# Kernel tuning notes

Measured on AMD Instinct MI355X. Metric: run time of the kernel, lower is better.

The kernel has to match this reference:

```python
import jax, jax.numpy as jnp
import numpy as np

B, PLEN, D = 32, 1024, 256


def setup_inputs() -> dict:
    key = jax.random.key(0)
    ks = jax.random.split(key, 8)
    u = lambda k, shape: jax.random.uniform(k, shape, jnp.float32, -0.05, 0.05)
    return {
        "P": jax.random.normal(ks[0], (B, PLEN, D), jnp.float32),
        "w_itr_att": u(ks[1], (3 * D,)),
        "w1": u(ks[2], (2 * D, D)),
        "w2": u(ks[3], (2 * D, D)),
        "w3": u(ks[4], (2 * D, D)),
        "b1": u(ks[5], (D,)),
        "b2": u(ks[6], (D,)),
        "b3": u(ks[7], (D,)),
    }


def reference(P, w_itr_att, w1, w2, w3, b1, b2, b3):
    d = P.shape[-1]
    # alpha(a,b) = w_itr_att . [a ; b ; a*b]; split w into the three d-chunks
    wa, wb, wc = w_itr_att[:d], w_itr_att[d:2 * d], w_itr_att[2 * d:]
    # pairwise score A[b,i,j] = wa.P_i + wb.P_j + wc.(P_i * P_j)
    sa = P @ wa                                   # (b, p)
    sb = P @ wb                                   # (b, p)
    A = sa[:, :, None] + sb[:, None, :] + jnp.einsum('bid,bjd->bij', P * wc, P)
    itr_attn = jnp.einsum('bij,bjd->bid', jax.nn.softmax(A, axis=2), P)
    cat = jnp.concatenate([P, itr_attn], axis=-1)  # (b, p, 2d)
    z = jnp.tanh(cat @ w1 + b1)
    r = jax.nn.sigmoid(cat @ w2 + b2)
    f = jax.nn.sigmoid(cat @ w3 + b3)
    return r * P + f * z
```

## Files before the change

### kernel.cpp

```cpp
#include <hip/hip_runtime.h>
#include <hip/hip_bf16.h>

typedef unsigned short u16;
typedef unsigned int   u32;
typedef unsigned char  u8;

using bf16x8 = __attribute__((ext_vector_type(8))) short;
using f32x4  = __attribute__((ext_vector_type(4))) float;

#define NB 32
#define NP 1024
#define ND 256

__device__ __forceinline__ u16 f2bf(float x){
  u32 u = __float_as_uint(x);
  u += 0x7FFFu + ((u >> 16) & 1u);
  return (u16)(u >> 16);
}

__device__ __forceinline__ float bf2f(u16 x){
  return __uint_as_float((u32)x << 16);
}

#if __has_builtin(__builtin_amdgcn_cvt_pk_fp8_f32)
template<bool HI>
__device__ __forceinline__ u32 pk_fp8(float a, float b, u32 old){
  return (u32)__builtin_amdgcn_cvt_pk_fp8_f32(a, b, (int)old, HI);
}
#else
__device__ __forceinline__ u8 f2e4m3(float x){
  u32 b = __float_as_uint(x);
  u32 s = (b >> 31) << 7;
  float ax = __uint_as_float(b & 0x7fffffffu);
  if (!(ax < 464.f)) return (u8)(s | 0x7E);
  if (ax < 0.001953125f) return (u8)s;
  if (ax < 0.015625f){
    u32 m = (u32)__float2int_rn(ax * 512.f);
    return (u8)(s | m);
  }
  u32 bb = b & 0x7fffffffu;
  bb += 0x7ffffu + ((bb >> 20) & 1u);
  int e = (int)(bb >> 23) - 127 + 7;
  u32 m = (bb >> 20) & 7u;
  if (e > 15 || (e == 15 && m == 7)) return (u8)(s | 0x7E);
  return (u8)(s | ((u32)e << 3) | m);
}
template<bool HI>
__device__ __forceinline__ u32 pk_fp8(float a, float b, u32 old){
  u32 v = (u32)f2e4m3(a) | ((u32)f2e4m3(b) << 8);
  return HI ? ((old & 0xFFFFu) | (v << 16)) : ((old & 0xFFFF0000u) | v);
}
#endif

__device__ __forceinline__ void glds16(const void* g, void* l){
  __builtin_amdgcn_global_load_lds((const __attribute__((address_space(1))) void*)g,
                                   (__attribute__((address_space(3))) void*)l, 16, 0, 0);
}

__global__ void prep_pt(const float* __restrict__ P, const float* __restrict__ wi,
                        u16* __restrict__ Pbf, u16* __restrict__ PbfT,
                        u8* __restrict__ P8, float* __restrict__ sbv){
  const int b = blockIdx.y, jt = blockIdx.x;
  __shared__ __align__(16) u16 T[64][264];
  const int tid = threadIdx.x;
  const int row = tid >> 2;
  const int dq  = tid & 3;
  const size_t grow = (size_t)b * NP + jt * 64 + row;
  const float* prow = P + grow * ND;
  const float* wbp  = wi + ND;
  float s = 0.f;
  #pragma unroll
  for (int it = 0; it < 4; ++it){
    const int d0 = it * 64 + dq * 16;
    float4 a0 = *(const float4*)(prow + d0);
    float4 a1 = *(const float4*)(prow + d0 + 4);
    float4 a2 = *(const float4*)(prow + d0 + 8);
    float4 a3 = *(const float4*)(prow + d0 + 12);
    float4 w0 = *(const float4*)(wbp + d0);
    float4 w1 = *(const float4*)(wbp + d0 + 4);
    float4 w2 = *(const float4*)(wbp + d0 + 8);
    float4 w3 = *(const float4*)(wbp + d0 + 12);
    s += a0.x*w0.x + a0.y*w0.y + a0.z*w0.z + a0.w*w0.w;
    s += a1.x*w1.x + a1.y*w1.y + a1.z*w1.z + a1.w*w1.w;
    s += a2.x*w2.x + a2.y*w2.y + a2.z*w2.z + a2.w*w2.w;
    s += a3.x*w3.x + a3.y*w3.y + a3.z*w3.z + a3.w*w3.w;
    u16 tmp[16];
    tmp[0]=f2bf(a0.x); tmp[1]=f2bf(a0.y); tmp[2]=f2bf(a0.z); tmp[3]=f2bf(a0.w);
    tmp[4]=f2bf(a1.x); tmp[5]=f2bf(a1.y); tmp[6]=f2bf(a1.z); tmp[7]=f2bf(a1.w);
    tmp[8]=f2bf(a2.x); tmp[9]=f2bf(a2.y); tmp[10]=f2bf(a2.z); tmp[11]=f2bf(a2.w);
    tmp[12]=f2bf(a3.x); tmp[13]=f2bf(a3.y); tmp[14]=f2bf(a3.z); tmp[15]=f2bf(a3.w);
    *(uint4*)&T[row][d0]     = *(uint4*)tmp;
    *(uint4*)&T[row][d0 + 8] = *(uint4*)(tmp + 8);
    *(uint4*)(Pbf + grow * ND + d0)     = *(uint4*)tmp;
    *(uint4*)(Pbf + grow * ND + d0 + 8) = *(uint4*)(tmp + 8);
    u32 q0 = pk_fp8<false>(a0.x, a0.y, 0); q0 = pk_fp8<true>(a0.z, a0.w, q0);
    u32 q1 = pk_fp8<false>(a1.x, a1.y, 0); q1 = pk_fp8<true>(a1.z, a1.w, q1);
    u32 q2 = pk_fp8<false>(a2.x, a2.y, 0); q2 = pk_fp8<true>(a2.z, a2.w, q2);
    u32 q3 = pk_fp8<false>(a3.x, a3.y, 0); q3 = pk_fp8<true>(a3.z, a3.w, q3);
    uint4 pq; pq.x = q0; pq.y = q1; pq.z = q2; pq.w = q3;
    *(uint4*)(P8 + grow * ND + d0) = pq;
  }
  s += __shfl_xor(s, 1, 64);
  s += __shfl_xor(s, 2, 64);
  if (dq == 0) sbv[grow] = s;
  __syncthreads();
  #pragma unroll
  for (int it = 0; it < 8; ++it){
    int cc = tid + 256 * it;
    int d = cc >> 3, c8 = cc & 7;
    u16 tmp[8];
    #pragma unroll
    for (int k = 0; k < 8; ++k) tmp[k] = T[c8 * 8 + k][d];
    *(uint4*)(PbfT + ((size_t)b * ND + d) * NP + jt * 64 + c8 * 8) = *(uint4*)tmp;
  }
}

__global__ void prep_w(const float* __restrict__ w1, const float* __restrict__ w2,
                       const float* __restrict__ w3, u16* __restrict__ Wp){
  const int t = blockIdx.x;
  const float* w = (t < 16) ? w1 : ((t < 32) ? w2 : w3);
  const int tid = threadIdx.x;
  #pragma unroll
  for (int j = 0; j < 4; ++j){
    int item = tid + 256 * j;
    int c = item >> 6, lane = item & 63;
    int ncol = ((t & 15) << 4) + (lane & 15);
    int k0 = 32 * c + 8 * (lane >> 4);
    u16 tmp[8];
    #pragma unroll
    for (int e = 0; e < 8; ++e) tmp[e] = f2bf(w[(size_t)(k0 + e) * 256 + ncol]);
    *(uint4*)(Wp + ((size_t)(t * 16 + c) * 64 + lane) * 8) = *(uint4*)tmp;
  }
}

__launch_bounds__(256, 2)
__global__ void attn_kernel(const float* __restrict__ P, const float* __restrict__ wi,
                            const u8* __restrict__ P8, const u16* __restrict__ PbfT,
                            const float* __restrict__ sbv, u16* __restrict__ attnb){
  const int p    = blockIdx.x;
  const int bid  = ((p & 7) << 6) | (p >> 3);
  const int b    = bid >> 4;
  const int q0   = (bid & 15) << 6;
  const int tid  = threadIdx.x;
  const int wave = tid >> 6, lane = tid & 63, lo = lane & 15, hi = lane >> 4;

  __shared__ __align__(16) u8  Kt8[64 * 256];
  __shared__ __align__(16) u16 VtA[256 * 64];
  __shared__ __align__(16) u16 Sp[4][16][72];
  __shared__ float sls[4][16];
  __shared__ float lfin[64];
  __shared__ u32 fastf[4];
  char* KtB = (char*)Kt8;
  char* VtB = (char*)VtA;

  long qf8[8];
  {
    const int qrow = q0 + wave * 16 + lo;
    const float* prow = P  + ((size_t)b * NP + qrow) * ND;
    const float* wcp  = wi + 512;
    #pragma unroll
    for (int c = 0; c < 8; ++c){
      const int d0 = 32 * c + 8 * hi;
      float4 a  = *(const float4*)(prow + d0);
      float4 a2 = *(const float4*)(prow + d0 + 4);
      float4 wa  = *(const float4*)(wcp + d0);
      float4 wa2 = *(const float4*)(wcp + d0 + 4);
      u32 w0 = pk_fp8<false>(16.f*a.x*wa.x,  16.f*a.y*wa.y,  0);
      w0     = pk_fp8<true >(16.f*a.z*wa.z,  16.f*a.w*wa.w,  w0);
      u32 w1 = pk_fp8<false>(16.f*a2.x*wa2.x, 16.f*a2.y*wa2.y, 0);
      w1     = pk_fp8<true >(16.f*a2.z*wa2.z, 16.f*a2.w*wa2.w, w1);
      qf8[c] = (long)(((unsigned long long)w1 << 32) | w0);
    }
  }

  f32x4 of[4][4];
  #pragma unroll
  for (int qt = 0; qt < 4; ++qt)
    #pragma unroll
    for (int dt = 0; dt < 4; ++dt) of[qt][dt] = (f32x4){0.f,0.f,0.f,0.f};
  float mx[4] = {-1e30f,-1e30f,-1e30f,-1e30f};
  float ls[4] = {0.f,0.f,0.f,0.f};

  const u8*  kslab = P8   + (size_t)b * NP * ND;
  const u16* vslab = PbfT + (size_t)b * ND * NP;

  auto stageK = [&](int kt){
    const int kbase = kt * 64;
    #pragma unroll
    for (int it = 0; it < 4; ++it){
      int off = it * 4096 + tid * 16;
      int j   = off >> 8;
      int u   = ((off >> 4) & 15) ^ (j & 7);
      glds16((const char*)(kslab + (size_t)(kbase + j) * ND + u * 16), KtB + off);
    }
  };
  auto stageV = [&](int kt){
    const int kbase = kt * 64;
    #pragma unroll
    for (int it = 0; it < 8; ++it){
      int off = it * 4096 + tid * 16;
      int d   = off >> 7;
      int kc  = ((off >> 4) & 7) ^ (d & 7);
      glds16((const char*)(vslab + (size_t)d * NP + kbase + kc * 8), VtB + off);
    }
  };

  float sbc[4], sbn[4];
  stageK(0);
  stageV(0);
  #pragma unroll
  for (int nt = 0; nt < 4; ++nt) sbc[nt] = sbv[(size_t)b * NP + nt * 16 + lo];
  __syncthreads();

  for (int kt = 0; kt < 16; ++kt){
    f32x4 s[4];
    #pragma unroll
    for (int nt = 0; nt < 4; ++nt){
      f32x4 acc = (f32x4){0.f,0.f,0.f,0.f};
      #pragma unroll
      for (int c = 0; c < 8; ++c){
        int j  = nt * 16 + lo;
        int ad = j * 256 + (((2 * c + (hi >> 1)) ^ (j & 7)) << 4) + 8 * (hi & 1);
        long kf8 = *(const long*)(KtB + ad);
        acc = __builtin_amdgcn_mfma_f32_16x16x32_fp8_fp8(qf8[c], kf8, acc, 0, 0, 0);
      }
      float sv = sbc[nt];
      #pragma unroll
      for (int r = 0; r < 4; ++r) s[nt][r] = fmaf(acc[r], 0.0625f, sv);
    }

    float scale[4] = {1.f, 1.f, 1.f, 1.f};
    int fast = 1;
    {
      float md = -1e30f;
      #pragma unroll
      for (int nt = 0; nt < 4; ++nt)
        #pragma unroll
        for (int r = 0; r < 4; ++r) md = fmaxf(md, s[nt][r] - mx[r]);
      if (!__all(md <= 8.f)){
        fast = 0;
        #pragma unroll
        for (int r = 0; r < 4; ++r){
          float v = fmaxf(fmaxf(s[0][r], s[1][r]), fmaxf(s[2][r], s[3][r]));
          v = fmaxf(v, __shfl_xor(v, 1, 64));
          v = fmaxf(v, __shfl_xor(v, 2, 64));
          v = fmaxf(v, __shfl_xor(v, 4, 64));
          v = fmaxf(v, __shfl_xor(v, 8, 64));
          float mnew = fmaxf(mx[r], v);
          scale[r] = __expf(mx[r] - mnew);
          mx[r] = mnew;
          ls[r] *= scale[r];
        }
      }
    }
    #pragma unroll
    for (int nt = 0; nt < 4; ++nt)
      #pragma unroll
      for (int r = 0; r < 4; ++r){
        float pv = __expf(s[nt][r] - mx[r]);
        ls[r] += pv;
        Sp[wave][4 * hi + r][16 * nt + lo] = f2bf(pv);
      }
    if (lane == 0) fastf[wave] = (u32)fast;
    if (lo == 0){
      #pragma unroll
      for (int r = 0; r < 4; ++r) sls[wave][4 * hi + r] = scale[r];
    }

    __syncthreads();
    if (kt < 15) stageK(kt + 1);

    if (!(fastf[0] & fastf[1] & fastf[2] & fastf[3])){
      #pragma unroll
      for (int qt = 0; qt < 4; ++qt){
        #pragma unroll
        for (int r = 0; r < 4; ++r){
          float sc = sls[qt][4 * hi + r];
          #pragma unroll
          for (int dt = 0; dt < 4; ++dt) of[qt][dt][r] *= sc;
        }
      }
    }

    #pragma unroll
    for (int kk = 0; kk < 2; ++kk){
      bf16x8 pa[4];
      #pragma unroll
      for (int qt = 0; qt < 4; ++qt)
        pa[qt] = *(const bf16x8*)&Sp[qt][lo][32 * kk + 8 * hi];
      #pragma unroll
      for (int dt = 0; dt < 4; ++dt){
        int d  = wave * 64 + dt * 16 + lo;
        int ad = d * 128 + (((4 * kk + hi) ^ (d & 7)) << 4);
        bf16x8 vb = *(const bf16x8*)(VtB + ad);
        #pragma unroll
        for (int qt = 0; qt < 4; ++qt)
          of[qt][dt] = __builtin_amdgcn_mfma_f32_16x16x32_bf16(pa[qt], vb, of[qt][dt], 0, 0, 0);
      }
    }

    __syncthreads();
    if (kt < 15){
      stageV(kt + 1);
      #pragma unroll
      for (int nt = 0; nt < 4; ++nt)
        sbn[nt] = sbv[(size_t)b * NP + (kt + 1) * 64 + nt * 16 + lo];
      sbc[0] = sbn[0]; sbc[1] = sbn[1]; sbc[2] = sbn[2]; sbc[3] = sbn[3];
    }
  }

  #pragma unroll
  for (int r = 0; r < 4; ++r){
    ls[r] += __shfl_xor(ls[r], 1, 64);
    ls[r] += __shfl_xor(ls[r], 2, 64);
    ls[r] += __shfl_xor(ls[r], 4, 64);
    ls[r] += __shfl_xor(ls[r], 8, 64);
  }
  if (lo == 0){
    #pragma unroll
    for (int r = 0; r < 4; ++r) lfin[wave * 16 + 4 * hi + r] = ls[r];
  }
  __syncthreads();
  #pragma unroll
  for (int qt = 0; qt < 4; ++qt){
    #pragma unroll
    for (int r = 0; r < 4; ++r){
      const float inv = 1.f / lfin[qt * 16 + 4 * hi + r];
      const int qrow = q0 + qt * 16 + 4 * hi + r;
      #pragma unroll
      for (int dt = 0; dt < 4; ++dt){
        float o = of[qt][dt][r] * inv;
        attnb[((size_t)b * NP + qrow) * ND + wave * 64 + dt * 16 + lo] = f2bf(o);
      }
    }
  }
}

__launch_bounds__(256, 2)
__global__ void mlp_kernel(const u16* __restrict__ Pbf, const u16* __restrict__ attnb,
                           const u16* __restrict__ Wp,
                           const float* __restrict__ b1, const float* __restrict__ b2,
                           const float* __restrict__ b3, float* __restrict__ out){
  const int p    = blockIdx.x;
  const int swz  = ((p & 7) << 7) | (p >> 3);
  const int mt   = swz >> 2, cg = swz & 3;
  const int tid  = threadIdx.x;
  const int wave = tid >> 6, lane = tid & 63, lo = lane & 15, hi = lane >> 4;
  const int tq   = 4 * cg + wave;
  const int m0   = mt * 128;

  __shared__ __align__(16) u16 Ab[2][128 * 64];

  f32x4 acc[3][8];
  #pragma unroll
  for (int e = 0; e < 3; ++e)
    #pragma unroll
    for (int m = 0; m < 8; ++m) acc[e][m] = (f32x4){0.f,0.f,0.f,0.f};

  auto stage = [&](int s, int buf){
    const u16* xs = (s < 4) ? (Pbf   + (size_t)m0 * ND + s * 64)
                            : (attnb + (size_t)m0 * ND + (s - 4) * 64);
    char* dst = (char*)Ab[buf];
    #pragma unroll
    for (int it = 0; it < 4; ++it){
      int off = it * 4096 + wave * 1024 + lane * 16;
      int row = off >> 7;
      int cl  = (off & 127) ^ ((row & 7) << 4);
      glds16((const char*)(xs + (size_t)row * ND) + cl, dst + it * 4096 + wave * 1024);
    }
  };

  stage(0, 0);
  __syncthreads();

  for (int s = 0; s < 8; ++s){
    if (s < 7) stage(s + 1, (s + 1) & 1);
    const char* ab = (const char*)Ab[s & 1];
    #pragma unroll
    for (int cc = 0; cc < 2; ++cc){
      const int c = 2 * s + cc;
      bf16x8 wf[3];
      #pragma unroll
      for (int e = 0; e < 3; ++e)
        wf[e] = *(const bf16x8*)(Wp + ((size_t)((tq + 16 * e) * 16 + c) * 64 + lane) * 8);
      #pragma unroll
      for (int m = 0; m < 8; ++m){
        int row = 16 * m + lo;
        bf16x8 af = *(const bf16x8*)(ab + row * 128 + ((64 * cc + 16 * hi) ^ ((row & 7) << 4)));
        #pragma unroll
        for (int e = 0; e < 3; ++e)
          acc[e][m] = __builtin_amdgcn_mfma_f32_16x16x32_bf16(af, wf[e], acc[e][m], 0, 0, 0);
      }
    }
    __syncthreads();
  }

  const int d = 16 * tq + lo;
  const float bb1 = b1[d], bb2 = b2[d], bb3 = b3[d];
  #pragma unroll
  for (int m = 0; m < 8; ++m){
    #pragma unroll
    for (int r = 0; r < 4; ++r){
      const int row = m0 + 16 * m + 4 * hi + r;
      float y1 = acc[0][m][r] + bb1;
      float y2 = acc[1][m][r] + bb2;
      float y3 = acc[2][m][r] + bb3;
      float pv = bf2f(Pbf[(size_t)row * ND + d]);
      float e2 = __expf(2.f * y1);
      float z  = (e2 - 1.f) / (e2 + 1.f);
      float rr = 1.f / (1.f + __expf(-y2));
      float ff = 1.f / (1.f + __expf(-y3));
      out[(size_t)row * ND + d] = rr * pv + ff * z;
    }
  }
}

extern "C" void kernel_launch(void* const* d_in, const int* in_sizes, int n_in,
                              void* d_out, int out_size, void* d_ws, size_t ws_size,
                              hipStream_t stream){
  const float* P  = (const float*)d_in[0];
  const float* wi = (const float*)d_in[1];
  const float* w1 = (const float*)d_in[2];
  const float* w2 = (const float*)d_in[3];
  const float* w3 = (const float*)d_in[4];
  const float* b1 = (const float*)d_in[5];
  const float* b2 = (const float*)d_in[6];
  const float* b3 = (const float*)d_in[7];
  float* out = (float*)d_out;

  char* ws = (char*)d_ws;
  u16*   Pbf   = (u16*)  (ws);
  u16*   PbfT  = (u16*)  (ws + (16u << 20));
  u16*   attnb = (u16*)  (ws + (32u << 20));
  u16*   Wp    = (u16*)  (ws + (48u << 20));
  float* sbv   = (float*)(ws + (49u << 20));
  u8*    P8    = (u8*)   (ws + (50u << 20));

  prep_pt<<<dim3(16, 32), 256, 0, stream>>>(P, wi, Pbf, PbfT, P8, sbv);
  prep_w<<<48, 256, 0, stream>>>(w1, w2, w3, Wp);
  attn_kernel<<<512, 256, 0, stream>>>(P, wi, P8, PbfT, sbv, attnb);
  mlp_kernel<<<1024, 256, 0, stream>>>(Pbf, attnb, Wp, b1, b2, b3, out);
}
```

Before: 108.0 us.

## Store attention output as fp8 and use fp8 MFMA for its half of the gate GEMM

The attention kernel now writes its normalized output as e4m3 fp8 bytes instead of bf16, halving that intermediate's write and read traffic. The matching half of the gate weights is prepacked as fp8 scaled by 16. The MLP kernel runs that K-half with fp8 MFMA, rescales the accumulators, then runs the P-half in bf16 as before. The residual term now reads P directly in fp32. This trades accuracy in the attention path for less memory traffic and cheaper matrix ops, and adds a second LDS buffer set.

```diff
diff --git a/kernel.cpp b/kernel.cpp
--- a/kernel.cpp
+++ b/kernel.cpp
@@ -22,12 +22,6 @@
   return __uint_as_float((u32)x << 16);
 }
 
-#if __has_builtin(__builtin_amdgcn_cvt_pk_fp8_f32)
-template<bool HI>
-__device__ __forceinline__ u32 pk_fp8(float a, float b, u32 old){
-  return (u32)__builtin_amdgcn_cvt_pk_fp8_f32(a, b, (int)old, HI);
-}
-#else
 __device__ __forceinline__ u8 f2e4m3(float x){
   u32 b = __float_as_uint(x);
   u32 s = (b >> 31) << 7;
@@ -45,11 +39,21 @@
   if (e > 15 || (e == 15 && m == 7)) return (u8)(s | 0x7E);
   return (u8)(s | ((u32)e << 3) | m);
 }
+#if __has_builtin(__builtin_amdgcn_cvt_pk_fp8_f32)
+template<bool HI>
+__device__ __forceinline__ u32 pk_fp8(float a, float b, u32 old){
+  return (u32)__builtin_amdgcn_cvt_pk_fp8_f32(a, b, (int)old, HI);
+}
+__device__ __forceinline__ u8 f8byte(float x){
+  return (u8)(pk_fp8<false>(x, 0.f, 0) & 0xFFu);
+}
+#else
 template<bool HI>
 __device__ __forceinline__ u32 pk_fp8(float a, float b, u32 old){
   u32 v = (u32)f2e4m3(a) | ((u32)f2e4m3(b) << 8);
   return HI ? ((old & 0xFFFFu) | (v << 16)) : ((old & 0xFFFF0000u) | v);
 }
+__device__ __forceinline__ u8 f8byte(float x){ return f2e4m3(x); }
 #endif
 
 __device__ __forceinline__ void glds16(const void* g, void* l){
@@ -116,7 +120,8 @@
 }
 
 __global__ void prep_w(const float* __restrict__ w1, const float* __restrict__ w2,
-                       const float* __restrict__ w3, u16* __restrict__ Wp){
+                       const float* __restrict__ w3,
+                       u16* __restrict__ Wp, u8* __restrict__ W8){
   const int t = blockIdx.x;
   const float* w = (t < 16) ? w1 : ((t < 32) ? w2 : w3);
   const int tid = threadIdx.x;
@@ -126,17 +131,26 @@
     int c = item >> 6, lane = item & 63;
     int ncol = ((t & 15) << 4) + (lane & 15);
     int k0 = 32 * c + 8 * (lane >> 4);
-    u16 tmp[8];
-    #pragma unroll
-    for (int e = 0; e < 8; ++e) tmp[e] = f2bf(w[(size_t)(k0 + e) * 256 + ncol]);
-    *(uint4*)(Wp + ((size_t)(t * 16 + c) * 64 + lane) * 8) = *(uint4*)tmp;
+    if (c < 8){
+      u16 tmp[8];
+      #pragma unroll
+      for (int e = 0; e < 8; ++e) tmp[e] = f2bf(w[(size_t)(k0 + e) * 256 + ncol]);
+      *(uint4*)(Wp + ((size_t)(t * 8 + c) * 64 + lane) * 8) = *(uint4*)tmp;
+    } else {
+      u32 lo32 = pk_fp8<false>(16.f * w[(size_t)(k0+0)*256+ncol], 16.f * w[(size_t)(k0+1)*256+ncol], 0);
+      lo32     = pk_fp8<true >(16.f * w[(size_t)(k0+2)*256+ncol], 16.f * w[(size_t)(k0+3)*256+ncol], lo32);
+      u32 hi32 = pk_fp8<false>(16.f * w[(size_t)(k0+4)*256+ncol], 16.f * w[(size_t)(k0+5)*256+ncol], 0);
+      hi32     = pk_fp8<true >(16.f * w[(size_t)(k0+6)*256+ncol], 16.f * w[(size_t)(k0+7)*256+ncol], hi32);
+      uint2 pv; pv.x = lo32; pv.y = hi32;
+      *(uint2*)(W8 + ((size_t)(t * 8 + (c - 8)) * 64 + lane) * 8) = pv;
+    }
   }
 }
 
 __launch_bounds__(256, 2)
 __global__ void attn_kernel(const float* __restrict__ P, const float* __restrict__ wi,
                             const u8* __restrict__ P8, const u16* __restrict__ PbfT,
-                            const float* __restrict__ sbv, u16* __restrict__ attnb){
+                            const float* __restrict__ sbv, u8* __restrict__ attnb8){
   const int p    = blockIdx.x;
   const int bid  = ((p & 7) << 6) | (p >> 3);
   const int b    = bid >> 4;
@@ -330,15 +344,16 @@
       #pragma unroll
       for (int dt = 0; dt < 4; ++dt){
         float o = of[qt][dt][r] * inv;
-        attnb[((size_t)b * NP + qrow) * ND + wave * 64 + dt * 16 + lo] = f2bf(o);
+        attnb8[((size_t)b * NP + qrow) * ND + wave * 64 + dt * 16 + lo] = f8byte(o);
       }
     }
   }
 }
 
 __launch_bounds__(256, 2)
-__global__ void mlp_kernel(const u16* __restrict__ Pbf, const u16* __restrict__ attnb,
-                           const u16* __restrict__ Wp,
+__global__ void mlp_kernel(const u16* __restrict__ Pbf, const u8* __restrict__ attnb8,
+                           const u16* __restrict__ Wp, const u8* __restrict__ W8,
+                           const float* __restrict__ Pf,
                            const float* __restrict__ b1, const float* __restrict__ b2,
                            const float* __restrict__ b3, float* __restrict__ out){
   const int p    = blockIdx.x;
@@ -349,7 +364,8 @@
   const int tq   = 4 * cg + wave;
   const int m0   = mt * 128;
 
-  __shared__ __align__(16) u16 Ab[2][128 * 64];
+  __shared__ __align__(16) u16 Ab16[2][128 * 64];
+  __shared__ __align__(16) u8  Ab8[2][128 * 64];
 
   f32x4 acc[3][8];
   #pragma unroll
@@ -357,32 +373,72 @@
     #pragma unroll
     for (int m = 0; m < 8; ++m) acc[e][m] = (f32x4){0.f,0.f,0.f,0.f};
 
-  auto stage = [&](int s, int buf){
-    const u16* xs = (s < 4) ? (Pbf   + (size_t)m0 * ND + s * 64)
-                            : (attnb + (size_t)m0 * ND + (s - 4) * 64);
-    char* dst = (char*)Ab[buf];
+  auto stage16 = [&](int s, int buf){
+    const u16* xs = Pbf + (size_t)m0 * ND + s * 64;
+    char* dst = (char*)Ab16[buf];
     #pragma unroll
     for (int it = 0; it < 4; ++it){
-      int off = it * 4096 + wave * 1024 + lane * 16;
+      int off = it * 4096 + tid * 16;
       int row = off >> 7;
       int cl  = (off & 127) ^ ((row & 7) << 4);
-      glds16((const char*)(xs + (size_t)row * ND) + cl, dst + it * 4096 + wave * 1024);
+      glds16((const char*)(xs + (size_t)row * ND) + cl, dst + off);
     }
   };
-
-  stage(0, 0);
+  auto stage8 = [&](int s, int buf){
+    const u8* xs = attnb8 + (size_t)m0 * ND + s * 64;
+    char* dst = (char*)Ab8[buf];
+    #pragma unroll
+    for (int it = 0; it < 2; ++it){
+      int off = it * 4096 + tid * 16;
+      int row = off >> 6;
+      int u   = ((off >> 4) & 3) ^ ((row >> 1) & 3);
+      glds16((const char*)(xs + (size_t)row * ND + u * 16), dst + off);
+    }
+  };
+
+  stage8(0, 0);
   __syncthreads();
-
-  for (int s = 0; s < 8; ++s){
-    if (s < 7) stage(s + 1, (s + 1) & 1);
-    const char* ab = (const char*)Ab[s & 1];
+  for (int s = 0; s < 4; ++s){
+    if (s < 3) stage8(s + 1, (s + 1) & 1);
+    else       stage16(0, 0);
+    const char* ab = (const char*)Ab8[s & 1];
+    #pragma unroll
+    for (int cc = 0; cc < 2; ++cc){
+      const int c = 2 * s + cc;
+      long wf8[3];
+      #pragma unroll
+      for (int e = 0; e < 3; ++e)
+        wf8[e] = *(const long*)(W8 + ((size_t)((tq + 16 * e) * 8 + c) * 64 + lane) * 8);
+      #pragma unroll
+      for (int m = 0; m < 8; ++m){
+        int row = 16 * m + lo;
+        int ad  = row * 64 + (((2 * cc + (hi >> 1)) ^ ((row >> 1) & 3)) << 4) + 8 * (hi & 1);
+        long af8 = *(const long*)(ab + ad);
+        #pragma unroll
+        for (int e = 0; e < 3; ++e)
+          acc[e][m] = __builtin_amdgcn_mfma_f32_16x16x32_fp8_fp8(af8, wf8[e], acc[e][m], 0, 0, 0);
+      }
+    }
+    __syncthreads();
+  }
+
+  #pragma unroll
+  for (int e = 0; e < 3; ++e)
+    #pragma unroll
+    for (int m = 0; m < 8; ++m)
+      #pragma unroll
+      for (int r = 0; r < 4; ++r) acc[e][m][r] *= 0.0625f;
+
+  for (int s = 0; s < 4; ++s){
+    if (s < 3) stage16(s + 1, (s + 1) & 1);
+    const char* ab = (const char*)Ab16[s & 1];
     #pragma unroll
     for (int cc = 0; cc < 2; ++cc){
       const int c = 2 * s + cc;
       bf16x8 wf[3];
       #pragma unroll
       for (int e = 0; e < 3; ++e)
-        wf[e] = *(const bf16x8*)(Wp + ((size_t)((tq + 16 * e) * 16 + c) * 64 + lane) * 8);
+        wf[e] = *(const bf16x8*)(Wp + ((size_t)((tq + 16 * e) * 8 + c) * 64 + lane) * 8);
       #pragma unroll
       for (int m = 0; m < 8; ++m){
         int row = 16 * m + lo;
@@ -405,7 +461,7 @@
       float y1 = acc[0][m][r] + bb1;
       float y2 = acc[1][m][r] + bb2;
       float y3 = acc[2][m][r] + bb3;
-      float pv = bf2f(Pbf[(size_t)row * ND + d]);
+      float pv = Pf[(size_t)row * ND + d];
       float e2 = __expf(2.f * y1);
       float z  = (e2 - 1.f) / (e2 + 1.f);
       float rr = 1.f / (1.f + __expf(-y2));
@@ -429,15 +485,16 @@
   float* out = (float*)d_out;
 
   char* ws = (char*)d_ws;
-  u16*   Pbf   = (u16*)  (ws);
-  u16*   PbfT  = (u16*)  (ws + (16u << 20));
-  u16*   attnb = (u16*)  (ws + (32u << 20));
+  u16*   PbfT  = (u16*)  (ws);
+  u8*    P8    = (u8*)   (ws + (16u << 20));
+  u8*    atn8  = (u8*)   (ws + (24u << 20));
+  u16*   Pbf   = (u16*)  (ws + (32u << 20));
   u16*   Wp    = (u16*)  (ws + (48u << 20));
+  u8*    W8    = (u8*)   (ws + (48u << 20) + 524288);
   float* sbv   = (float*)(ws + (49u << 20));
-  u8*    P8    = (u8*)   (ws + (50u << 20));
 
   prep_pt<<<dim3(16, 32), 256, 0, stream>>>(P, wi, Pbf, PbfT, P8, sbv);
-  prep_w<<<48, 256, 0, stream>>>(w1, w2, w3, Wp);
-  attn_kernel<<<512, 256, 0, stream>>>(P, wi, P8, PbfT, sbv, attnb);
-  mlp_kernel<<<1024, 256, 0, stream>>>(Pbf, attnb, Wp, b1, b2, b3, out);
-}
+  prep_w<<<48, 256, 0, stream>>>(w1, w2, w3, Wp, W8);
+  attn_kernel<<<512, 256, 0, stream>>>(P, wi, P8, PbfT, sbv, atn8);
+  mlp_kernel<<<1024, 256, 0, stream>>>(Pbf, atn8, Wp, W8, P, b1, b2, b3, out);
+}
```

Result: no change. 109.1 us (+0.9%).
